# Optimization experiments

Hardware: AMD Instinct MI355X
Metric: run time of the kernel (lower is better)

The kernel has to match this reference:

```python
import jax, jax.numpy as jnp
import numpy as np

B = 1024
X_DIM = 64
X_SPARSE_DIM = 32
SPARSE_EMB_DIM = 8
S_SEQ_DIM = 32
S_DIM = 16
Y_DIM = 1
H = 64
F = X_DIM + X_SPARSE_DIM * SPARSE_EMB_DIM + S_SEQ_DIM  # 352
FC1_IN = F + 2 * S_DIM  # 384


def setup_inputs() -> dict:
    key = jax.random.key(0)
    ks = jax.random.split(key, 40)
    g = lambda i, shape: jax.random.normal(ks[i], shape, dtype=jnp.float32) * 0.05
    return {
        'X': jax.random.normal(ks[0], (B, X_DIM), dtype=jnp.float32),
        'X_sparse': jax.random.normal(ks[1], (B, X_SPARSE_DIM), dtype=jnp.float32),
        'X_seq': jax.random.normal(ks[2], (B, S_SEQ_DIM), dtype=jnp.float32),
        'S': jax.random.normal(ks[3], (B, S_DIM), dtype=jnp.float32),
        'R': jax.random.normal(ks[4], (B, S_DIM), dtype=jnp.float32),
        'sparse_emb_w': g(5, (X_SPARSE_DIM, SPARSE_EMB_DIM)),
        'x_rep_w': g(6, (F, H)),
        'Qw': g(7, (H, H)), 'Qb': g(8, (H,)),
        'Kw': g(9, (H, H)), 'Kb': g(10, (H,)),
        'Vw': g(11, (H, H)), 'Vb': g(12, (H,)),
        'ws1': g(13, (H, 1)), 'bs1': g(14, (H,)),
        'wx2': g(15, (H, F)), 'bx2': g(16, (H,)),
        'wsx33': g(17, (1, H)), 'bsx33': g(18, (1,)),
        'wr1': g(19, (H, 1)), 'br1': g(20, (H,)),
        'wxx2': g(21, (H, F)), 'bxx2': g(22, (H,)),
        'wrx33': g(23, (1, H)), 'brx33': g(24, (1,)),
        'fc1w': g(25, (H, FC1_IN)), 'fc1b': g(26, (H,)),
        'fc2w': g(27, (H, H)), 'fc2b': g(28, (H,)),
        'fc3w': g(29, (Y_DIM, H)), 'fc3b': g(30, (Y_DIM,)),
    }


def _interaction_attn(s, x, w1, b1, w2, b2, w33, b33):
    # vectorized version of the per-feature Python loop over s_dim
    # h_s: [B, s_dim, H] = sigmoid(Linear(1->H)(s_i)) for each feature i
    h_s = jax.nn.sigmoid(s[:, :, None] * w1[:, 0][None, None, :] + b1)
    h_x = jax.nn.sigmoid(x @ w2.T + b2)                  # [B, H]
    h = jax.nn.relu(h_s + h_x[:, None, :])               # [B, s_dim, H]
    score = jnp.einsum('bsh,h->bs', h, w33[0]) + b33[0]  # [B, s_dim]
    attn = jax.nn.softmax(score, axis=1)
    return s * attn, attn


def reference(X, X_sparse, X_seq, S, R, sparse_emb_w, x_rep_w,
              Qw, Qb, Kw, Kb, Vw, Vb,
              ws1, bs1, wx2, bx2, wsx33, bsx33,
              wr1, br1, wxx2, bxx2, wrx33, brx33,
              fc1w, fc1b, fc2w, fc2b, fc3w, fc3b):
    # sparse outer-product embedding -> flatten
    Xs = (X_sparse[:, :, None] * sparse_emb_w[None]).reshape(X.shape[0], -1)
    Xc = jnp.concatenate([X, Xs, X_seq], axis=1)          # [B, F]
    # per-feature representation via outer product with embedding table
    X_rep = Xc[:, :, None] * x_rep_w[None]                # [B, F, H]
    Xn = X_rep / jnp.linalg.norm(X_rep, axis=1, keepdims=True)
    # feature-wise self-attention
    Q = jnp.einsum('bfd,ed->bfe', Xn, Qw) + Qb
    K = jnp.einsum('bfd,ed->bfe', Xn, Kw) + Kb
    V = jnp.einsum('bfd,ed->bfe', Xn, Vw) + Vb
    scores = jnp.einsum('bfe,bge->bfg', Q, K) / jnp.sqrt(jnp.float32(H))
    attn = jax.nn.softmax(scores, axis=-1)                # [B, F, F]
    _ = jnp.einsum('bfg,bge->bfe', attn, V)               # xx (unused downstream)
    X_attn_feature = jnp.einsum('bf,bfg->bg', Xc, attn)   # [B, F]
    sx, _ = _interaction_attn(S, Xc, ws1, bs1, wx2, bx2, wsx33, bsx33)
    rx, _ = _interaction_attn(R, Xc, wr1, br1, wxx2, bxx2, wrx33, brx33)
    x = jnp.concatenate([X_attn_feature, sx, rx], axis=1)
    x = jax.nn.relu(x @ fc1w.T + fc1b)
    x = jax.nn.relu(x @ fc2w.T + fc2b)
    return x @ fc3w.T + fc3b
```

## Files before the change

### kernel.cpp

```cpp
#include <hip/hip_runtime.h>
#include <hip/hip_bf16.h>

#define BATCH 1024
#define FDIM  352
#define FPAD  384
#define HDIM  64

typedef short bf16x8 __attribute__((ext_vector_type(8)));
typedef float f32x4  __attribute__((ext_vector_type(4)));
typedef unsigned short ushort_t;

__device__ __forceinline__ ushort_t f2bf(float x) {
    union { float f; unsigned u; } v; v.f = x;
    unsigned u = v.u;
    unsigned r = u + 0x7FFFu + ((u >> 16) & 1u);
    return (ushort_t)(r >> 16);
}

__device__ __forceinline__ float sigmoidf_(float x) {
    return 1.0f / (1.0f + __expf(-x));
}

__global__ void prep_kernel(const float* __restrict__ xrepw, ushort_t* __restrict__ wbf) {
    int idx = blockIdx.x * 256 + threadIdx.x;
    if (idx < FPAD * 64) {
        int f = idx >> 6;
        wbf[idx] = (f < FDIM) ? f2bf(xrepw[idx]) : (ushort_t)0;
    }
}

__global__ __launch_bounds__(256, 2) void fused_model(
    const float* __restrict__ X,    const float* __restrict__ Xsp,  const float* __restrict__ Xseq,
    const float* __restrict__ S,    const float* __restrict__ R,
    const float* __restrict__ emb,  const float* __restrict__ xrepw,
    const float* __restrict__ Qw,   const float* __restrict__ Qb,
    const float* __restrict__ Kw,   const float* __restrict__ Kb,
    const float* __restrict__ ws1,  const float* __restrict__ bs1,
    const float* __restrict__ wx2,  const float* __restrict__ bx2,
    const float* __restrict__ wsx33,const float* __restrict__ bsx33,
    const float* __restrict__ wr1,  const float* __restrict__ br1,
    const float* __restrict__ wxx2, const float* __restrict__ bxx2,
    const float* __restrict__ wrx33,const float* __restrict__ brx33,
    const float* __restrict__ fc1w, const float* __restrict__ fc1b,
    const float* __restrict__ fc2w, const float* __restrict__ fc2b,
    const float* __restrict__ fc3w, const float* __restrict__ fc3b,
    const ushort_t* __restrict__ wbf, float* __restrict__ out)
{
    __shared__ __align__(16) ushort_t klds[FPAD * 64];
    __shared__ __align__(16) ushort_t scr[4][16 * 64];
    __shared__ float xc[FPAD];
    __shared__ float rnorm[HDIM];
    __shared__ float qbs[HDIM], kbs[HDIM];
    __shared__ float outa[FPAD];
    __shared__ float hx[2][HDIM];
    __shared__ float a1[HDIM], a2[HDIM];

    const int b  = blockIdx.x;
    const int t  = threadIdx.x;
    const int l  = t & 63;
    const int wv = t >> 6;

    for (int f = t; f < FPAD; f += 256) {
        float v;
        if (f < 64)       v = X[b * 64 + f];
        else if (f < 320) { int i = (f - 64) >> 3, j = (f - 64) & 7; v = Xsp[b * 32 + i] * emb[i * 8 + j]; }
        else if (f < 352) v = Xseq[b * 32 + (f - 320)];
        else              v = 0.f;
        xc[f]   = v;
        outa[f] = 0.f;
    }
    if (t < HDIM) { qbs[t] = Qb[t]; kbs[t] = Kb[t]; }
    __syncthreads();

    {
        const int d = t & 63, q = t >> 6;
        float acc = 0.f;
        for (int f = q; f < FDIM; f += 4) {
            float v = xc[f] * xrepw[f * 64 + d];
            acc = fmaf(v, v, acc);
        }
        float* pf = (float*)scr;
        pf[q * 64 + d] = acc;
        __syncthreads();
        if (t < 64) {
            float n2 = pf[t] + pf[64 + t] + pf[128 + t] + pf[192 + t];
            rnorm[t] = rsqrtf(n2);
        }
        __syncthreads();
    }

    bf16x8 bq[4][2], bk[4][2];
    {
        const int kg = l >> 4;
        #pragma unroll
        for (int n = 0; n < 4; ++n) {
            const int ee = n * 16 + (l & 15);
            #pragma unroll
            for (int s = 0; s < 2; ++s) {
                const int d0 = s * 32 + kg * 8;
                bf16x8 vq, vk;
                #pragma unroll
                for (int j = 0; j < 8; ++j) {
                    float rn = rnorm[d0 + j];
                    vq[j] = (short)f2bf(rn * Qw[ee * 64 + d0 + j]);
                    vk[j] = (short)f2bf(rn * Kw[ee * 64 + d0 + j]);
                }
                bq[n][s] = vq; bk[n][s] = vk;
            }
        }
    }

    bf16x8 aq[6][2];
    {
        const int row = l & 15;
        const int kg  = l >> 4;
        #pragma unroll
        for (int im = 0; im < 6; ++im) {
            const int f0 = (wv * 6 + im) * 16;
            bf16x8 aw[2];
            #pragma unroll
            for (int s = 0; s < 2; ++s)
                aw[s] = *reinterpret_cast<const bf16x8*>(&wbf[(f0 + row) * 64 + s * 32 + kg * 8]);

            f32x4 pq[4], pk[4];
            #pragma unroll
            for (int n = 0; n < 4; ++n) { pq[n] = (f32x4){0.f,0.f,0.f,0.f}; pk[n] = (f32x4){0.f,0.f,0.f,0.f}; }
            #pragma unroll
            for (int s = 0; s < 2; ++s) {
                #pragma unroll
                for (int n = 0; n < 4; ++n) {
                    pq[n] = __builtin_amdgcn_mfma_f32_16x16x32_bf16(aw[s], bq[n][s], pq[n], 0, 0, 0);
                    pk[n] = __builtin_amdgcn_mfma_f32_16x16x32_bf16(aw[s], bk[n][s], pk[n], 0, 0, 0);
                }
            }
            const int fr0 = kg * 4;
            float xcr[4];
            #pragma unroll
            for (int r = 0; r < 4; ++r) xcr[r] = xc[f0 + fr0 + r];
            #pragma unroll
            for (int n = 0; n < 4; ++n) {
                const int e = n * 16 + (l & 15);
                const float qbe = qbs[e], kbe = kbs[e];
                #pragma unroll
                for (int r = 0; r < 4; ++r) {
                    const int f  = f0 + fr0 + r;
                    const int fr = fr0 + r;
                    klds[f * 64 + (e ^ ((f & 7) << 3))]      = f2bf(fmaf(xcr[r], pk[n][r], kbe));
                    scr[wv][fr * 64 + (e ^ ((fr & 7) << 3))] = f2bf(fmaf(xcr[r], pq[n][r], qbe));
                }
            }
            asm volatile("s_waitcnt lgkmcnt(0)" ::: "memory");
            __builtin_amdgcn_sched_barrier(0);
            #pragma unroll
            for (int s = 0; s < 2; ++s)
                aq[im][s] = *reinterpret_cast<const bf16x8*>(
                    &scr[wv][row * 64 + ((s * 32 + kg * 8) ^ ((row & 7) << 3))]);
            asm volatile("s_waitcnt lgkmcnt(0)" ::: "memory");
            __builtin_amdgcn_sched_barrier(0);
        }
    }
    __syncthreads();

    {
        const int row = l & 15;
        const int kg  = l >> 4;
        #pragma unroll
        for (int im = 0; im < 6; ++im) {
            const int f0 = (wv * 6 + im) * 16;
            f32x4 acc[22];
            #pragma unroll
            for (int nt = 0; nt < 22; ++nt) {
                const int g = nt * 16 + row;
                bf16x8 b0 = *reinterpret_cast<const bf16x8*>(&klds[g * 64 + ((kg * 8)      ^ ((g & 7) << 3))]);
                bf16x8 b1 = *reinterpret_cast<const bf16x8*>(&klds[g * 64 + ((32 + kg * 8) ^ ((g & 7) << 3))]);
                f32x4 a = (f32x4){0.f,0.f,0.f,0.f};
                a = __builtin_amdgcn_mfma_f32_16x16x32_bf16(aq[im][0], b0, a, 0, 0, 0);
                a = __builtin_amdgcn_mfma_f32_16x16x32_bf16(aq[im][1], b1, a, 0, 0, 0);
                acc[nt] = a;
            }
            float m[4] = {-1e30f, -1e30f, -1e30f, -1e30f};
            #pragma unroll
            for (int nt = 0; nt < 22; ++nt) {
                #pragma unroll
                for (int r = 0; r < 4; ++r) {
                    float s = acc[nt][r] * 0.125f;
                    acc[nt][r] = s;
                    m[r] = fmaxf(m[r], s);
                }
            }
            #pragma unroll
            for (int r = 0; r < 4; ++r) {
                #pragma unroll
                for (int off = 1; off < 16; off <<= 1)
                    m[r] = fmaxf(m[r], __shfl_xor(m[r], off, 64));
            }
            float lsum[4] = {0.f, 0.f, 0.f, 0.f};
            #pragma unroll
            for (int nt = 0; nt < 22; ++nt) {
                #pragma unroll
                for (int r = 0; r < 4; ++r) {
                    float p = __expf(acc[nt][r] - m[r]);
                    acc[nt][r] = p;
                    lsum[r] += p;
                }
            }
            #pragma unroll
            for (int r = 0; r < 4; ++r) {
                #pragma unroll
                for (int off = 1; off < 16; off <<= 1)
                    lsum[r] += __shfl_xor(lsum[r], off, 64);
            }
            float coef[4];
            #pragma unroll
            for (int r = 0; r < 4; ++r) coef[r] = xc[f0 + kg * 4 + r] / lsum[r];
            #pragma unroll
            for (int nt = 0; nt < 22; ++nt) {
                float po = coef[0]*acc[nt][0] + coef[1]*acc[nt][1] + coef[2]*acc[nt][2] + coef[3]*acc[nt][3];
                po += __shfl_xor(po, 16, 64);
                po += __shfl_xor(po, 32, 64);
                if (l < 16) atomicAdd(&outa[nt * 16 + l], po);
            }
        }
    }
    __syncthreads();

    if (wv < 2) {
        const float* w2 = (wv == 0) ? wx2 : wxx2;
        const float* b2 = (wv == 0) ? bx2 : bxx2;
        const int fo = l & 3;
        const int hb = l >> 2;
        float acc[4] = {0.f, 0.f, 0.f, 0.f};
        for (int f = fo; f < FDIM; f += 4) {
            float xv = xc[f];
            #pragma unroll
            for (int c = 0; c < 4; ++c)
                acc[c] = fmaf(xv, w2[(hb + 16 * c) * FDIM + f], acc[c]);
        }
        #pragma unroll
        for (int c = 0; c < 4; ++c) {
            acc[c] += __shfl_xor(acc[c], 1, 64);
            acc[c] += __shfl_xor(acc[c], 2, 64);
        }
        if (fo == 0) {
            #pragma unroll
            for (int c = 0; c < 4; ++c) {
                int h = hb + 16 * c;
                hx[wv][h] = sigmoidf_(acc[c] + b2[h]);
            }
        }
    }
    __syncthreads();

    if (wv < 2) {
        const float* sv  = (wv == 0) ? S     : R;
        const float* w1  = (wv == 0) ? ws1   : wr1;
        const float* b1  = (wv == 0) ? bs1   : br1;
        const float* w33 = (wv == 0) ? wsx33 : wrx33;
        const float  b33 = (wv == 0) ? bsx33[0] : brx33[0];
        const float w1h = w1[l], b1h = b1[l], w33h = w33[l], hxh = hx[wv][l];
        float myscore = 0.f;
        for (int i = 0; i < 16; ++i) {
            float s  = sv[b * 16 + i];
            float hs = sigmoidf_(fmaf(s, w1h, b1h));
            float v  = fmaxf(hs + hxh, 0.f) * w33h;
            #pragma unroll
            for (int off = 1; off < 64; off <<= 1) v += __shfl_xor(v, off, 64);
            if (i == l) myscore = v + b33;
        }
        float mm = myscore;
        #pragma unroll
        for (int off = 1; off < 16; off <<= 1) mm = fmaxf(mm, __shfl_xor(mm, off, 64));
        float p  = __expf(myscore - mm);
        float ss = p;
        #pragma unroll
        for (int off = 1; off < 16; off <<= 1) ss += __shfl_xor(ss, off, 64);
        if (l < 16) outa[FDIM + wv * 16 + l] = sv[b * 16 + l] * (p / ss);
    }
    __syncthreads();

    {
        const int h = t >> 2, jo = t & 3;
        float acc = 0.f;
        for (int j = jo; j < 384; j += 4)
            acc = fmaf(outa[j], fc1w[h * 384 + j], acc);
        acc += __shfl_xor(acc, 1, 64);
        acc += __shfl_xor(acc, 2, 64);
        if (jo == 0) a1[h] = fmaxf(acc + fc1b[h], 0.f);
    }
    __syncthreads();
    {
        const int h = t >> 2, jo = t & 3;
        float acc = 0.f;
        #pragma unroll
        for (int j = jo; j < 64; j += 4)
            acc = fmaf(a1[j], fc2w[h * 64 + j], acc);
        acc += __shfl_xor(acc, 1, 64);
        acc += __shfl_xor(acc, 2, 64);
        if (jo == 0) a2[h] = fmaxf(acc + fc2b[h], 0.f);
    }
    __syncthreads();
    if (wv == 0) {
        float v = fc3w[l] * a2[l];
        #pragma unroll
        for (int off = 1; off < 64; off <<= 1) v += __shfl_xor(v, off, 64);
        if (l == 0) out[b] = v + fc3b[0];
    }
}

extern "C" void kernel_launch(void* const* d_in, const int* in_sizes, int n_in,
                              void* d_out, int out_size, void* d_ws, size_t ws_size,
                              hipStream_t stream) {
    const float* X     = (const float*)d_in[0];
    const float* Xsp   = (const float*)d_in[1];
    const float* Xseq  = (const float*)d_in[2];
    const float* S     = (const float*)d_in[3];
    const float* R     = (const float*)d_in[4];
    const float* emb   = (const float*)d_in[5];
    const float* xrepw = (const float*)d_in[6];
    const float* Qw    = (const float*)d_in[7];
    const float* Qb    = (const float*)d_in[8];
    const float* Kw    = (const float*)d_in[9];
    const float* Kb    = (const float*)d_in[10];
    const float* ws1   = (const float*)d_in[13];
    const float* bs1   = (const float*)d_in[14];
    const float* wx2   = (const float*)d_in[15];
    const float* bx2   = (const float*)d_in[16];
    const float* wsx33 = (const float*)d_in[17];
    const float* bsx33 = (const float*)d_in[18];
    const float* wr1   = (const float*)d_in[19];
    const float* br1   = (const float*)d_in[20];
    const float* wxx2  = (const float*)d_in[21];
    const float* bxx2  = (const float*)d_in[22];
    const float* wrx33 = (const float*)d_in[23];
    const float* brx33 = (const float*)d_in[24];
    const float* fc1w  = (const float*)d_in[25];
    const float* fc1b  = (const float*)d_in[26];
    const float* fc2w  = (const float*)d_in[27];
    const float* fc2b  = (const float*)d_in[28];
    const float* fc3w  = (const float*)d_in[29];
    const float* fc3b  = (const float*)d_in[30];

    ushort_t* wbf = (ushort_t*)d_ws;

    prep_kernel<<<(FPAD * 64 + 255) / 256, 256, 0, stream>>>(xrepw, wbf);
    fused_model<<<BATCH, 256, 0, stream>>>(
        X, Xsp, Xseq, S, R, emb, xrepw,
        Qw, Qb, Kw, Kb,
        ws1, bs1, wx2, bx2, wsx33, bsx33,
        wr1, br1, wxx2, bxx2, wrx33, brx33,
        fc1w, fc1b, fc2w, fc2b, fc3w, fc3b,
        wbf, (float*)d_out);
}
```

Baseline: 311.3 us.

## Fold Q and K projections into a single bilinear form to shrink attention-score work

```diff
diff --git a/kernel.cpp b/kernel.cpp
--- a/kernel.cpp
+++ b/kernel.cpp
@@ -3,8 +3,8 @@
 
 #define BATCH 1024
 #define FDIM  352
-#define FPAD  384
 #define HDIM  64
+#define NT    22
 
 typedef short bf16x8 __attribute__((ext_vector_type(8)));
 typedef float f32x4  __attribute__((ext_vector_type(4)));
@@ -21,20 +21,46 @@
     return 1.0f / (1.0f + __expf(-x));
 }
 
-__global__ void prep_kernel(const float* __restrict__ xrepw, ushort_t* __restrict__ wbf) {
+__global__ void prep_w(const float* __restrict__ xrepw, ushort_t* __restrict__ wbf) {
     int idx = blockIdx.x * 256 + threadIdx.x;
-    if (idx < FPAD * 64) {
-        int f = idx >> 6;
-        wbf[idx] = (f < FDIM) ? f2bf(xrepw[idx]) : (ushort_t)0;
-    }
-}
-
-__global__ __launch_bounds__(256, 2) void fused_model(
+    if (idx < FDIM * HDIM) wbf[idx] = f2bf(xrepw[idx]);
+}
+
+__global__ void prep_m(const float* __restrict__ Qw, const float* __restrict__ Qb,
+                       const float* __restrict__ Kw, const float* __restrict__ Kb,
+                       float* __restrict__ MT, float* __restrict__ u0,
+                       float* __restrict__ v0, float* __restrict__ cS) {
+    __shared__ float qs[4096], ks[4096];
+    const int t = threadIdx.x, blk = blockIdx.x;
+    for (int i = t; i < 4096; i += 256) { qs[i] = Qw[i]; ks[i] = Kw[i]; }
+    __syncthreads();
+    if (blk < 16) {
+        int idx = blk * 256 + t;
+        int h = idx >> 6, d = idx & 63;
+        float acc = 0.f;
+        for (int e = 0; e < 64; ++e) acc = fmaf(qs[e * 64 + d], ks[e * 64 + h], acc);
+        MT[h * 64 + d] = acc;
+    } else {
+        if (t < 64) {
+            float a = 0.f;
+            for (int e = 0; e < 64; ++e) a = fmaf(qs[e * 64 + t], Kb[e], a);
+            u0[t] = a;
+        } else if (t < 128) {
+            int d = t - 64; float a = 0.f;
+            for (int e = 0; e < 64; ++e) a = fmaf(ks[e * 64 + d], Qb[e], a);
+            v0[d] = a;
+        } else if (t == 128) {
+            float a = 0.f;
+            for (int e = 0; e < 64; ++e) a = fmaf(Qb[e], Kb[e], a);
+            cS[0] = a;
+        }
+    }
+}
+
+__global__ __launch_bounds__(256, 3) void fused_model(
     const float* __restrict__ X,    const float* __restrict__ Xsp,  const float* __restrict__ Xseq,
     const float* __restrict__ S,    const float* __restrict__ R,
     const float* __restrict__ emb,  const float* __restrict__ xrepw,
-    const float* __restrict__ Qw,   const float* __restrict__ Qb,
-    const float* __restrict__ Kw,   const float* __restrict__ Kb,
     const float* __restrict__ ws1,  const float* __restrict__ bs1,
     const float* __restrict__ wx2,  const float* __restrict__ bx2,
     const float* __restrict__ wsx33,const float* __restrict__ bsx33,
@@ -44,146 +70,151 @@
     const float* __restrict__ fc1w, const float* __restrict__ fc1b,
     const float* __restrict__ fc2w, const float* __restrict__ fc2b,
     const float* __restrict__ fc3w, const float* __restrict__ fc3b,
-    const ushort_t* __restrict__ wbf, float* __restrict__ out)
+    const ushort_t* __restrict__ wbf, const float* __restrict__ MT,
+    const float* __restrict__ u0g,  const float* __restrict__ v0g,
+    const float* __restrict__ cS,   float* __restrict__ out)
 {
-    __shared__ __align__(16) ushort_t klds[FPAD * 64];
-    __shared__ __align__(16) ushort_t scr[4][16 * 64];
-    __shared__ float xc[FPAD];
+    __shared__ __align__(16) ushort_t plds[FDIM * 64];
+    __shared__ float xc[FDIM];
+    __shared__ float pu[FDIM], pv[FDIM];
+    __shared__ float outa[384];
     __shared__ float rnorm[HDIM];
-    __shared__ float qbs[HDIM], kbs[HDIM];
-    __shared__ float outa[FPAD];
     __shared__ float hx[2][HDIM];
+    __shared__ float ph[4][HDIM];
     __shared__ float a1[HDIM], a2[HDIM];
 
-    const int b  = blockIdx.x;
-    const int t  = threadIdx.x;
-    const int l  = t & 63;
-    const int wv = t >> 6;
-
-    for (int f = t; f < FPAD; f += 256) {
+    const int b   = blockIdx.x;
+    const int t   = threadIdx.x;
+    const int l   = t & 63;
+    const int wv  = t >> 6;
+    const int row = l & 15;
+    const int kg  = l >> 4;
+
+    for (int f = t; f < FDIM; f += 256) {
         float v;
         if (f < 64)       v = X[b * 64 + f];
         else if (f < 320) { int i = (f - 64) >> 3, j = (f - 64) & 7; v = Xsp[b * 32 + i] * emb[i * 8 + j]; }
-        else if (f < 352) v = Xseq[b * 32 + (f - 320)];
-        else              v = 0.f;
-        xc[f]   = v;
-        outa[f] = 0.f;
-    }
-    if (t < HDIM) { qbs[t] = Qb[t]; kbs[t] = Kb[t]; }
-    __syncthreads();
-
-    {
-        const int d = t & 63, q = t >> 6;
+        else              v = Xseq[b * 32 + (f - 320)];
+        xc[f] = v;
+    }
+    for (int f = t; f < 384; f += 256) outa[f] = 0.f;
+    __syncthreads();
+
+    {
         float acc = 0.f;
-        for (int f = q; f < FDIM; f += 4) {
-            float v = xc[f] * xrepw[f * 64 + d];
+        for (int f = wv; f < FDIM; f += 4) {
+            float v = xc[f] * xrepw[f * 64 + l];
             acc = fmaf(v, v, acc);
         }
-        float* pf = (float*)scr;
-        pf[q * 64 + d] = acc;
+        float* pf = &ph[0][0];
+        pf[wv * 64 + l] = acc;
         __syncthreads();
-        if (t < 64) {
-            float n2 = pf[t] + pf[64 + t] + pf[128 + t] + pf[192 + t];
-            rnorm[t] = rsqrtf(n2);
-        }
+        if (t < 64) rnorm[t] = rsqrtf(pf[t] + pf[64 + t] + pf[128 + t] + pf[192 + t]);
         __syncthreads();
     }
 
-    bf16x8 bq[4][2], bk[4][2];
-    {
-        const int kg = l >> 4;
+    bf16x8 bm[5][2];
+    {
+        float rd[16];
+        #pragma unroll
+        for (int s = 0; s < 2; ++s)
+            #pragma unroll
+            for (int j = 0; j < 8; ++j)
+                rd[s * 8 + j] = rnorm[s * 32 + kg * 8 + j];
         #pragma unroll
         for (int n = 0; n < 4; ++n) {
-            const int ee = n * 16 + (l & 15);
+            const float rh = rnorm[n * 16 + row] * 0.125f;
             #pragma unroll
             for (int s = 0; s < 2; ++s) {
-                const int d0 = s * 32 + kg * 8;
-                bf16x8 vq, vk;
-                #pragma unroll
-                for (int j = 0; j < 8; ++j) {
-                    float rn = rnorm[d0 + j];
-                    vq[j] = (short)f2bf(rn * Qw[ee * 64 + d0 + j]);
-                    vk[j] = (short)f2bf(rn * Kw[ee * 64 + d0 + j]);
+                const f32x4* mp = (const f32x4*)&MT[(n * 16 + row) * 64 + s * 32 + kg * 8];
+                f32x4 m0 = mp[0], m1 = mp[1];
+                bf16x8 v;
+                #pragma unroll
+                for (int j = 0; j < 4; ++j) {
+                    v[j]     = (short)f2bf(rd[s * 8 + j]     * m0[j] * rh);
+                    v[j + 4] = (short)f2bf(rd[s * 8 + j + 4] * m1[j] * rh);
                 }
-                bq[n][s] = vq; bk[n][s] = vk;
-            }
-        }
-    }
-
-    bf16x8 aq[6][2];
-    {
-        const int row = l & 15;
-        const int kg  = l >> 4;
-        #pragma unroll
-        for (int im = 0; im < 6; ++im) {
-            const int f0 = (wv * 6 + im) * 16;
-            bf16x8 aw[2];
-            #pragma unroll
-            for (int s = 0; s < 2; ++s)
-                aw[s] = *reinterpret_cast<const bf16x8*>(&wbf[(f0 + row) * 64 + s * 32 + kg * 8]);
-
-            f32x4 pq[4], pk[4];
-            #pragma unroll
-            for (int n = 0; n < 4; ++n) { pq[n] = (f32x4){0.f,0.f,0.f,0.f}; pk[n] = (f32x4){0.f,0.f,0.f,0.f}; }
-            #pragma unroll
-            for (int s = 0; s < 2; ++s) {
-                #pragma unroll
-                for (int n = 0; n < 4; ++n) {
-                    pq[n] = __builtin_amdgcn_mfma_f32_16x16x32_bf16(aw[s], bq[n][s], pq[n], 0, 0, 0);
-                    pk[n] = __builtin_amdgcn_mfma_f32_16x16x32_bf16(aw[s], bk[n][s], pk[n], 0, 0, 0);
+                bm[n][s] = v;
+            }
+        }
+        #pragma unroll
+        for (int s = 0; s < 2; ++s) {
+            bf16x8 v = {0, 0, 0, 0, 0, 0, 0, 0};
+            if (row < 2) {
+                const float* src = (row == 0) ? u0g : v0g;
+                const f32x4* up = (const f32x4*)&src[s * 32 + kg * 8];
+                f32x4 a0 = up[0], a1v = up[1];
+                #pragma unroll
+                for (int j = 0; j < 4; ++j) {
+                    v[j]     = (short)f2bf(rd[s * 8 + j]     * a0[j]  * 0.125f);
+                    v[j + 4] = (short)f2bf(rd[s * 8 + j + 4] * a1v[j] * 0.125f);
                 }
             }
-            const int fr0 = kg * 4;
-            float xcr[4];
-            #pragma unroll
-            for (int r = 0; r < 4; ++r) xcr[r] = xc[f0 + fr0 + r];
-            #pragma unroll
-            for (int n = 0; n < 4; ++n) {
-                const int e = n * 16 + (l & 15);
-                const float qbe = qbs[e], kbe = kbs[e];
+            bm[4][s] = v;
+        }
+    }
+
+    for (int mt = wv; mt < NT; mt += 4) {
+        const int f0 = mt * 16;
+        const bf16x8 aw0 = *(const bf16x8*)&wbf[(f0 + row) * 64 + kg * 8];
+        const bf16x8 aw1 = *(const bf16x8*)&wbf[(f0 + row) * 64 + 32 + kg * 8];
+        f32x4 p[5];
+        #pragma unroll
+        for (int n = 0; n < 5; ++n) {
+            f32x4 a = {0.f, 0.f, 0.f, 0.f};
+            a = __builtin_amdgcn_mfma_f32_16x16x32_bf16(aw0, bm[n][0], a, 0, 0, 0);
+            a = __builtin_amdgcn_mfma_f32_16x16x32_bf16(aw1, bm[n][1], a, 0, 0, 0);
+            p[n] = a;
+        }
+        #pragma unroll
+        for (int r = 0; r < 4; ++r) {
+            const int f = f0 + kg * 4 + r;
+            const int sw = (f & 7) << 3;
+            #pragma unroll
+            for (int n = 0; n < 4; ++n)
+                plds[f * 64 + ((n * 16 + row) ^ sw)] = f2bf(p[n][r]);
+            if (row == 0)      pu[f] = p[4][r];
+            else if (row == 1) pv[f] = p[4][r];
+        }
+    }
+    __syncthreads();
+
+    {
+        const float cg = cS[0] * 0.125f;
+        for (int mt = wv; mt < NT; mt += 4) {
+            const int f0 = mt * 16;
+            const int swr = (row & 7) << 3;
+            const bf16x8 ap0 = *(const bf16x8*)&plds[(f0 + row) * 64 + ((kg * 8) ^ swr)];
+            const bf16x8 ap1 = *(const bf16x8*)&plds[(f0 + row) * 64 + ((32 + kg * 8) ^ swr)];
+
+            f32x4 acc[NT];
+            #pragma unroll
+            for (int nt = 0; nt < NT; ++nt) {
+                const int g = nt * 16 + row;
+                bf16x8 b0 = *(const bf16x8*)&wbf[g * 64 + kg * 8];
+                bf16x8 b1 = *(const bf16x8*)&wbf[g * 64 + 32 + kg * 8];
+                f32x4 a = {0.f, 0.f, 0.f, 0.f};
+                a = __builtin_amdgcn_mfma_f32_16x16x32_bf16(ap0, b0, a, 0, 0, 0);
+                a = __builtin_amdgcn_mfma_f32_16x16x32_bf16(ap1, b1, a, 0, 0, 0);
+                acc[nt] = a;
+            }
+
+            float xf[4], uf[4];
+            #pragma unroll
+            for (int r = 0; r < 4; ++r) {
+                const int f = f0 + kg * 4 + r;
+                xf[r] = xc[f];
+                uf[r] = fmaf(xf[r], pu[f], cg);
+            }
+            float m[4] = {-1e30f, -1e30f, -1e30f, -1e30f};
+            #pragma unroll
+            for (int nt = 0; nt < NT; ++nt) {
+                const int g = nt * 16 + row;
+                const float xg = xc[g];
+                const float vg = xg * pv[g];
                 #pragma unroll
                 for (int r = 0; r < 4; ++r) {
-                    const int f  = f0 + fr0 + r;
-                    const int fr = fr0 + r;
-                    klds[f * 64 + (e ^ ((f & 7) << 3))]      = f2bf(fmaf(xcr[r], pk[n][r], kbe));
-                    scr[wv][fr * 64 + (e ^ ((fr & 7) << 3))] = f2bf(fmaf(xcr[r], pq[n][r], qbe));
-                }
-            }
-            asm volatile("s_waitcnt lgkmcnt(0)" ::: "memory");
-            __builtin_amdgcn_sched_barrier(0);
-            #pragma unroll
-            for (int s = 0; s < 2; ++s)
-                aq[im][s] = *reinterpret_cast<const bf16x8*>(
-                    &scr[wv][row * 64 + ((s * 32 + kg * 8) ^ ((row & 7) << 3))]);
-            asm volatile("s_waitcnt lgkmcnt(0)" ::: "memory");
-            __builtin_amdgcn_sched_barrier(0);
-        }
-    }
-    __syncthreads();
-
-    {
-        const int row = l & 15;
-        const int kg  = l >> 4;
-        #pragma unroll
-        for (int im = 0; im < 6; ++im) {
-            const int f0 = (wv * 6 + im) * 16;
-            f32x4 acc[22];
-            #pragma unroll
-            for (int nt = 0; nt < 22; ++nt) {
-                const int g = nt * 16 + row;
-                bf16x8 b0 = *reinterpret_cast<const bf16x8*>(&klds[g * 64 + ((kg * 8)      ^ ((g & 7) << 3))]);
-                bf16x8 b1 = *reinterpret_cast<const bf16x8*>(&klds[g * 64 + ((32 + kg * 8) ^ ((g & 7) << 3))]);
-                f32x4 a = (f32x4){0.f,0.f,0.f,0.f};
-                a = __builtin_amdgcn_mfma_f32_16x16x32_bf16(aq[im][0], b0, a, 0, 0, 0);
-                a = __builtin_amdgcn_mfma_f32_16x16x32_bf16(aq[im][1], b1, a, 0, 0, 0);
-                acc[nt] = a;
-            }
-            float m[4] = {-1e30f, -1e30f, -1e30f, -1e30f};
-            #pragma unroll
-            for (int nt = 0; nt < 22; ++nt) {
-                #pragma unroll
-                for (int r = 0; r < 4; ++r) {
-                    float s = acc[nt][r] * 0.125f;
+                    float s = fmaf(xf[r] * xg, acc[nt][r], uf[r] + vg);
                     acc[nt][r] = s;
                     m[r] = fmaxf(m[r], s);
                 }
@@ -196,7 +227,7 @@
             }
             float lsum[4] = {0.f, 0.f, 0.f, 0.f};
             #pragma unroll
-            for (int nt = 0; nt < 22; ++nt) {
+            for (int nt = 0; nt < NT; ++nt) {
                 #pragma unroll
                 for (int r = 0; r < 4; ++r) {
                     float p = __expf(acc[nt][r] - m[r]);
@@ -212,10 +243,11 @@
             }
             float coef[4];
             #pragma unroll
-            for (int r = 0; r < 4; ++r) coef[r] = xc[f0 + kg * 4 + r] / lsum[r];
-            #pragma unroll
-            for (int nt = 0; nt < 22; ++nt) {
-                float po = coef[0]*acc[nt][0] + coef[1]*acc[nt][1] + coef[2]*acc[nt][2] + coef[3]*acc[nt][3];
+            for (int r = 0; r < 4; ++r) coef[r] = xf[r] / lsum[r];
+            #pragma unroll
+            for (int nt = 0; nt < NT; ++nt) {
+                float po = coef[0] * acc[nt][0] + coef[1] * acc[nt][1]
+                         + coef[2] * acc[nt][2] + coef[3] * acc[nt][3];
                 po += __shfl_xor(po, 16, 64);
                 po += __shfl_xor(po, 32, 64);
                 if (l < 16) atomicAdd(&outa[nt * 16 + l], po);
@@ -224,14 +256,14 @@
     }
     __syncthreads();
 
-    if (wv < 2) {
-        const float* w2 = (wv == 0) ? wx2 : wxx2;
-        const float* b2 = (wv == 0) ? bx2 : bxx2;
-        const int fo = l & 3;
-        const int hb = l >> 2;
+    {
+        const int br = wv >> 1, fh = wv & 1;
+        const float* w2 = br ? wxx2 : wx2;
+        const int fo = l & 3, hb = l >> 2;
         float acc[4] = {0.f, 0.f, 0.f, 0.f};
-        for (int f = fo; f < FDIM; f += 4) {
-            float xv = xc[f];
+        for (int k = 0; k < 44; ++k) {
+            const int f = fh * 176 + fo + k * 4;
+            const float xv = xc[f];
             #pragma unroll
             for (int c = 0; c < 4; ++c)
                 acc[c] = fmaf(xv, w2[(hb + 16 * c) * FDIM + f], acc[c]);
@@ -243,38 +275,42 @@
         }
         if (fo == 0) {
             #pragma unroll
-            for (int c = 0; c < 4; ++c) {
-                int h = hb + 16 * c;
-                hx[wv][h] = sigmoidf_(acc[c] + b2[h]);
-            }
-        }
+            for (int c = 0; c < 4; ++c) ph[wv][hb + 16 * c] = acc[c];
+        }
+    }
+    __syncthreads();
+    if (t < 128) {
+        const int br = t >> 6, h = t & 63;
+        const float* b2 = br ? bxx2 : bx2;
+        hx[br][h] = sigmoidf_(ph[br * 2][h] + ph[br * 2 + 1][h] + b2[h]);
     }
     __syncthreads();
 
     if (wv < 2) {
-        const float* sv  = (wv == 0) ? S     : R;
-        const float* w1  = (wv == 0) ? ws1   : wr1;
-        const float* b1  = (wv == 0) ? bs1   : br1;
-        const float* w33 = (wv == 0) ? wsx33 : wrx33;
-        const float  b33 = (wv == 0) ? bsx33[0] : brx33[0];
-        const float w1h = w1[l], b1h = b1[l], w33h = w33[l], hxh = hx[wv][l];
-        float myscore = 0.f;
-        for (int i = 0; i < 16; ++i) {
-            float s  = sv[b * 16 + i];
-            float hs = sigmoidf_(fmaf(s, w1h, b1h));
-            float v  = fmaxf(hs + hxh, 0.f) * w33h;
-            #pragma unroll
-            for (int off = 1; off < 64; off <<= 1) v += __shfl_xor(v, off, 64);
-            if (i == l) myscore = v + b33;
-        }
-        float mm = myscore;
-        #pragma unroll
-        for (int off = 1; off < 16; off <<= 1) mm = fmaxf(mm, __shfl_xor(mm, off, 64));
-        float p  = __expf(myscore - mm);
+        const float* sv  = wv ? R     : S;
+        const float* w1  = wv ? wr1   : ws1;
+        const float* b1  = wv ? br1   : bs1;
+        const float* w33 = wv ? wrx33 : wsx33;
+        const float  b33 = wv ? brx33[0] : bsx33[0];
+        const int i = l >> 2, ho = l & 3;
+        const float si = sv[b * 16 + i];
+        float v = 0.f;
+        for (int k = 0; k < 16; ++k) {
+            const int h = ho * 16 + k;
+            float hs = sigmoidf_(fmaf(si, w1[h], b1[h]));
+            v = fmaf(fmaxf(hs + hx[wv][h], 0.f), w33[h], v);
+        }
+        v += __shfl_xor(v, 1, 64);
+        v += __shfl_xor(v, 2, 64);
+        const float sc = v + b33;
+        float mm = sc;
+        #pragma unroll
+        for (int off = 4; off < 64; off <<= 1) mm = fmaxf(mm, __shfl_xor(mm, off, 64));
+        const float p = __expf(sc - mm);
         float ss = p;
         #pragma unroll
-        for (int off = 1; off < 16; off <<= 1) ss += __shfl_xor(ss, off, 64);
-        if (l < 16) outa[FDIM + wv * 16 + l] = sv[b * 16 + l] * (p / ss);
+        for (int off = 4; off < 64; off <<= 1) ss += __shfl_xor(ss, off, 64);
+        if (ho == 0) outa[FDIM + wv * 16 + i] = si * (p / ss);
     }
     __syncthreads();
 
@@ -340,14 +376,19 @@
     const float* fc3w  = (const float*)d_in[29];
     const float* fc3b  = (const float*)d_in[30];
 
-    ushort_t* wbf = (ushort_t*)d_ws;
-
-    prep_kernel<<<(FPAD * 64 + 255) / 256, 256, 0, stream>>>(xrepw, wbf);
+    char* ws = (char*)d_ws;
+    ushort_t* wbf = (ushort_t*)(ws);
+    float*    MTp = (float*)(ws + 45056);
+    float*    u0  = (float*)(ws + 61440);
+    float*    v0  = (float*)(ws + 61696);
+    float*    cS  = (float*)(ws + 61952);
+
+    prep_w<<<(FDIM * HDIM + 255) / 256, 256, 0, stream>>>(xrepw, wbf);
+    prep_m<<<17, 256, 0, stream>>>(Qw, Qb, Kw, Kb, MTp, u0, v0, cS);
     fused_model<<<BATCH, 256, 0, stream>>>(
         X, Xsp, Xseq, S, R, emb, xrepw,
-        Qw, Qb, Kw, Kb,
         ws1, bs1, wx2, bx2, wsx33, bsx33,
         wr1, br1, wxx2, bxx2, wrx33, brx33,
         fc1w, fc1b, fc2w, fc2b, fc3w, fc3b,
-        wbf, (float*)d_out);
-}
+        wbf, MTp, u0, v0, cS, (float*)d_out);
+}
```

New measurement: 540.4 us. 73.6% more time.
